# Optimization experiments

Measured on AMD Instinct MI355X. Metric: run time of the kernel, lower is better.

Reference implementation:

```python
import jax, jax.numpy as jnp
import numpy as np

B, NE, NO, D = 8, 1024, 8, 1024
E, K, H = 8, 2, 2048          # num_experts, top-k, expert hidden
O = 1024                      # output_dim
NH, HD = 8, O // 8            # cross-attn heads, head dim
FH = 4 * O                    # ffn hidden


def setup_inputs() -> dict:
    key = jax.random.key(0)
    ks = jax.random.split(key, 24)
    s = lambda i, shape, fan: jax.random.normal(ks[i], shape, jnp.float32) * (1.0 / np.sqrt(fan))
    return {
        "x": jax.random.normal(ks[0], (B, NE, NO, D), jnp.float32),
        "attn_w": s(1, (D,), D),                 # Linear(D,1,bias=False)
        "gate_W": s(2, (D, E), D), "gate_b": jnp.zeros((E,), jnp.float32),
        "eW1": s(3, (E, D, H), D), "eb1": jnp.zeros((E, H), jnp.float32),
        "eW2": s(4, (E, H, O), H), "eb2": jnp.zeros((E, O), jnp.float32),
        "Wq": s(5, (O, O), O), "bq": jnp.zeros((O,), jnp.float32),
        "Wk": s(6, (O, O), O), "bk": jnp.zeros((O,), jnp.float32),
        "Wv": s(7, (O, O), O), "bv": jnp.zeros((O,), jnp.float32),
        "Wo": s(8, (O, O), O), "bo": jnp.zeros((O,), jnp.float32),
        "fW1": s(9, (O, FH), O), "fb1": jnp.zeros((FH,), jnp.float32),
        "fW2": s(10, (FH, O), FH), "fb2": jnp.zeros((O,), jnp.float32),
    }


def reference(x, attn_w, gate_W, gate_b, eW1, eb1, eW2, eb2,
              Wq, bq, Wk, bk, Wv, bv, Wo, bo, fW1, fb1, fW2, fb2):
    # 1) entity-level attention pooling over objects
    logits = jnp.einsum("bnod,d->bno", x, attn_w)          # (B,NE,NO)
    w = jax.nn.softmax(logits, axis=2)
    x_agg = jnp.einsum("bnod,bno->bnd", x, w)              # (B,NE,D)
    xt = x_agg.reshape(B * NE, D)                          # tokens

    # 2) MoE: top-k sparse routing + expert MLPs
    probs = jax.nn.softmax(xt @ gate_W + gate_b, axis=-1)  # (T,E)
    topv, topi = jax.lax.top_k(probs, K)
    gates = topv / jnp.sum(topv, axis=-1, keepdims=True)   # renormalize top-k
    T = xt.shape[0]
    w_full = jnp.zeros((T, E), xt.dtype).at[jnp.arange(T)[:, None], topi].set(gates)
    moe_out = jnp.zeros((T, O), xt.dtype)
    for e in range(E):  # small fixed loop over experts
        h = jax.nn.relu(xt @ eW1[e] + eb1[e])
        moe_out = moe_out + w_full[:, e:e + 1] * (h @ eW2[e] + eb2[e])
    ent = moe_out.reshape(B, NE, O)

    # 3) cross-attention (context=None -> self-attention)
    def split(t):
        return t.reshape(B, NE, NH, HD).transpose(0, 2, 1, 3)
    q = split(ent @ Wq + bq)
    k = split(ent @ Wk + bk)
    v = split(ent @ Wv + bv)
    scores = jnp.einsum("bhnd,bhmd->bhnm", q, k) / np.sqrt(HD).astype(np.float32)
    attn = jax.nn.softmax(scores, axis=-1)
    ctx = jnp.einsum("bhnm,bhmd->bhnd", attn, v)
    rel = ctx.transpose(0, 2, 1, 3).reshape(B, NE, O) @ Wo + bo

    # 4) FFN (dropout is identity in eval)
    return jax.nn.relu(rel @ fW1 + fb1) @ fW2 + fb2
```

## Files before the change

### kernel.cpp

```cpp
#include <hip/hip_runtime.h>
#include <hip/hip_bf16.h>
#include <math.h>


typedef __bf16 bf16_t;
typedef __bf16 bf16x8 __attribute__((ext_vector_type(8)));
typedef float  f32x4  __attribute__((ext_vector_type(4)));

#define B_   8
#define NE_  1024
#define NO_  8
#define D_   1024
#define E_   8
#define H_   2048
#define O_   1024
#define NH_  8
#define HD_  128
#define FH_  4096
#define T_   8192
#define NRB_ 32
#define NBLK_ 136
#define SLOTS_ (NBLK_*128)

__device__ __forceinline__ void gl2lds16(const bf16_t* g, bf16_t* l) {
    __builtin_amdgcn_global_load_lds(
        (const __attribute__((address_space(1))) unsigned int*)g,
        (__attribute__((address_space(3))) unsigned int*)l,
        16, 0, 0);
}

template<typename OUT_T, bool TRANSC, bool BIAS, bool RELU, bool GROUPED, bool GATHER>
__global__ __launch_bounds__(256, 2)
void gemm_nt(const bf16_t* __restrict__ A, const bf16_t* __restrict__ Bm,
             OUT_T* __restrict__ C,
             const float* __restrict__ bias,
             const int* __restrict__ rowidx, const int* __restrict__ blkexp,
             int K, int lda, int ldb, int ldc, float alpha, int zbase,
             long sBe, int biasStride,
             long sAb, long sAh, long sAz,
             long sBb, long sBh, long sBz,
             long sCb, long sCh, long sCz)
{
    const int z  = blockIdx.z;
    const long bh = zbase + z;
    const long bb = bh >> 3, hh = bh & 7;
    A  += bb*sAb + hh*sAh + (long)z*sAz;
    Bm += bb*sBb + hh*sBh + (long)z*sBz;
    C  += bb*sCb + hh*sCh + (long)z*sCz;

    if (GROUPED) {
        const int ge = blkexp[blockIdx.x];
        if (ge < 0) return;
        Bm += (long)ge * sBe;
        if (BIAS) bias += (long)ge * biasStride;
    }

    __shared__ __align__(16) bf16_t As[128*32];
    __shared__ __align__(16) bf16_t Bs[128*32];

    const int t    = threadIdx.x;
    const int lane = t & 63, wave = t >> 6;
    const int l16  = lane & 15, quad = lane >> 4;
    const int wm   = (wave & 1) * 64, wn = (wave >> 1) * 64;
    const int rowBase = blockIdx.x * 128;
    const int colBase = blockIdx.y * 128;

    const int lrow = lane >> 2;
    const int lch  = (lane & 3) * 8;
    long arow0, arow1;
    if (GATHER) {
        arow0 = rowidx[rowBase + wave*16 + lrow];
        arow1 = rowidx[rowBase + wave*16 + lrow + 64];
    } else {
        arow0 = rowBase + wave*16 + lrow;
        arow1 = arow0 + 64;
    }
    const bf16_t* agp0 = A  + arow0*lda + lch;
    const bf16_t* agp1 = A  + arow1*lda + lch;
    const bf16_t* bgp0 = Bm + (long)(colBase + wave*16 + lrow)*ldb + lch;
    const bf16_t* bgp1 = bgp0 + (long)64*ldb;
    bf16_t* alp0 = &As[wave*512];
    bf16_t* alp1 = &As[(4 + wave)*512];
    bf16_t* blp0 = &Bs[wave*512];
    bf16_t* blp1 = &Bs[(4 + wave)*512];

    f32x4 acc[4][4] = {};

    for (int k0 = 0; k0 < K; k0 += 32) {
        __syncthreads();
        gl2lds16(agp0 + k0, alp0);
        gl2lds16(agp1 + k0, alp1);
        gl2lds16(bgp0 + k0, blp0);
        gl2lds16(bgp1 + k0, blp1);
        __syncthreads();

        bf16x8 af[4], bfr[4];
        #pragma unroll
        for (int mi = 0; mi < 4; mi++)
            af[mi] = *(const bf16x8*)&As[(wm + mi*16 + l16)*32 + quad*8];
        #pragma unroll
        for (int ni = 0; ni < 4; ni++)
            bfr[ni] = *(const bf16x8*)&Bs[(wn + ni*16 + l16)*32 + quad*8];
        #pragma unroll
        for (int mi = 0; mi < 4; mi++)
            #pragma unroll
            for (int ni = 0; ni < 4; ni++)
                acc[mi][ni] = __builtin_amdgcn_mfma_f32_16x16x32_bf16(
                                  af[mi], bfr[ni], acc[mi][ni], 0, 0, 0);
    }

    #pragma unroll
    for (int mi = 0; mi < 4; mi++) {
        #pragma unroll
        for (int ni = 0; ni < 4; ni++) {
            const int col = colBase + wn + ni*16 + l16;
            float bv = 0.0f;
            if (BIAS) bv = bias[col];
            #pragma unroll
            for (int rr = 0; rr < 4; rr++) {
                const int row = rowBase + wm + mi*16 + quad*4 + rr;
                float v = acc[mi][ni][rr] * alpha;
                if (BIAS)   v += bv;
                if (RELU)   v = fmaxf(v, 0.0f);
                if (TRANSC) C[(long)col*ldc + row] = (OUT_T)v;
                else        C[(long)row*ldc + col] = (OUT_T)v;
            }
        }
    }
}

__global__ __launch_bounds__(256)
void transpose_convert(const float* __restrict__ in, bf16_t* __restrict__ out,
                       int R, int C, long inStride, long outStride)
{
    __shared__ float tl[64][65];
    const int t = threadIdx.x;
    const float* src = in  + (long)blockIdx.z * inStride;
    bf16_t*      dst = out + (long)blockIdx.z * outStride;
    const int c0 = blockIdx.x * 64, r0 = blockIdx.y * 64;
    #pragma unroll
    for (int i = 0; i < 16; i++) {
        const int idx = t + i*256, r = idx >> 6, c = idx & 63;
        tl[r][c] = src[(long)(r0 + r)*C + c0 + c];
    }
    __syncthreads();
    #pragma unroll
    for (int i = 0; i < 16; i++) {
        const int idx = t + i*256, rT = idx >> 6, cT = idx & 63;
        dst[(long)(c0 + rT)*R + r0 + cT] = (bf16_t)tl[cT][rT];
    }
}

__global__ __launch_bounds__(256)
void pool_kernel(const float* __restrict__ x, const float* __restrict__ attn_w,
                 float* __restrict__ xaggf, bf16_t* __restrict__ xaggb)
{
    __shared__ float xs[8192];
    __shared__ float red[32];
    const int t = threadIdx.x;
    const long tok = blockIdx.x;
    const float4* src = (const float4*)(x + tok*8192);
    float4* xs4 = (float4*)xs;
    #pragma unroll
    for (int i = 0; i < 8; i++) xs4[t + i*256] = src[t + i*256];
    float wreg[4];
    #pragma unroll
    for (int j = 0; j < 4; j++) wreg[j] = attn_w[t + j*256];
    __syncthreads();

    float part[8];
    #pragma unroll
    for (int o = 0; o < 8; o++) {
        float p = 0.0f;
        #pragma unroll
        for (int j = 0; j < 4; j++) p += xs[o*1024 + t + j*256] * wreg[j];
        part[o] = p;
    }
    const int lane = t & 63, wv = t >> 6;
    #pragma unroll
    for (int o = 0; o < 8; o++) {
        float v = part[o];
        for (int off = 32; off; off >>= 1) v += __shfl_down(v, off);
        if (lane == 0) red[o*4 + wv] = v;
    }
    __syncthreads();
    float lg[8], mx = -3.4e38f;
    #pragma unroll
    for (int o = 0; o < 8; o++) {
        lg[o] = red[o*4] + red[o*4+1] + red[o*4+2] + red[o*4+3];
        mx = fmaxf(mx, lg[o]);
    }
    float ssum = 0.0f;
    #pragma unroll
    for (int o = 0; o < 8; o++) { lg[o] = expf(lg[o] - mx); ssum += lg[o]; }
    const float inv = 1.0f / ssum;
    #pragma unroll
    for (int j = 0; j < 4; j++) {
        const int d = t + j*256;
        float a = 0.0f;
        #pragma unroll
        for (int o = 0; o < 8; o++) a += lg[o] * xs[o*1024 + d];
        a *= inv;
        xaggf[tok*1024 + d] = a;
        xaggb[tok*1024 + d] = (bf16_t)a;
    }
}

__global__ __launch_bounds__(256)
void gate_kernel(const float* __restrict__ xaggf, const float* __restrict__ gate_W,
                 const float* __restrict__ gate_b, float* __restrict__ gpair,
                 unsigned int* __restrict__ picks)
{
    const int t = threadIdx.x;
    const int lane = t & 63, wv = t >> 6;
    const long tok = (long)blockIdx.x*4 + wv;
    const float* xr = xaggf + tok*1024;
    float acc[8] = {0,0,0,0,0,0,0,0};
    for (int j = 0; j < 16; j++) {
        const int d = lane + j*64;
        const float xv = xr[d];
        const float4 w0 = *(const float4*)(gate_W + (long)d*8);
        const float4 w1 = *(const float4*)(gate_W + (long)d*8 + 4);
        acc[0] += xv*w0.x; acc[1] += xv*w0.y; acc[2] += xv*w0.z; acc[3] += xv*w0.w;
        acc[4] += xv*w1.x; acc[5] += xv*w1.y; acc[6] += xv*w1.z; acc[7] += xv*w1.w;
    }
    #pragma unroll
    for (int e = 0; e < 8; e++)
        for (int off = 32; off; off >>= 1) acc[e] += __shfl_down(acc[e], off);
    if (lane == 0) {
        float l[8];
        #pragma unroll
        for (int e = 0; e < 8; e++) l[e] = acc[e] + gate_b[e];
        int i1 = 0; float v1 = l[0];
        #pragma unroll
        for (int e = 1; e < 8; e++) if (l[e] > v1) { v1 = l[e]; i1 = e; }
        int i2 = -1; float v2 = -3.4e38f;
        #pragma unroll
        for (int e = 0; e < 8; e++) if (e != i1 && l[e] > v2) { v2 = l[e]; i2 = e; }
        const float tt = expf(v2 - v1);
        gpair[tok*2 + 0] = 1.0f/(1.0f + tt);
        gpair[tok*2 + 1] = tt/(1.0f + tt);
        picks[tok] = (unsigned)(i1 | (i2 << 8));
    }
}

__global__ __launch_bounds__(256)
void route_count(const unsigned int* __restrict__ picks, int* __restrict__ blockcnt)
{
    __shared__ int h[8];
    const int t = threadIdx.x;
    if (t < 8) h[t] = 0;
    __syncthreads();
    const unsigned p = picks[blockIdx.x*256 + t];
    atomicAdd(&h[p & 7], 1);
    atomicAdd(&h[(p >> 8) & 7], 1);
    __syncthreads();
    if (t < 8) blockcnt[blockIdx.x*8 + t] = h[t];
}

__global__ __launch_bounds__(256)
void route_offsets(const int* __restrict__ blockcnt,
                   int* __restrict__ blockbase, int* __restrict__ blkexp)
{
    __shared__ int cntS[8], eoffS[9];
    const int t = threadIdx.x;
    if (t < 8) {
        int s = 0;
        for (int b = 0; b < NRB_; b++) s += blockcnt[b*8 + t];
        cntS[t] = s;
    }
    __syncthreads();
    if (t == 0) {
        int r = 0;
        for (int e = 0; e < 8; e++) { eoffS[e] = r; r += (cntS[e] + 127) & ~127; }
        eoffS[8] = r;
    }
    __syncthreads();
    if (t < 8) {
        int r = eoffS[t];
        for (int b = 0; b < NRB_; b++) { blockbase[b*8 + t] = r; r += blockcnt[b*8 + t]; }
    }
    if (t < NBLK_) {
        const int s = t * 128;
        int e = -1;
        for (int q = 0; q < 8; q++) if (s >= eoffS[q] && s < eoffS[q+1]) e = q;
        blkexp[t] = e;
    }
}

__global__ __launch_bounds__(256)
void route_scatter(const unsigned int* __restrict__ picks,
                   const int* __restrict__ blockbase,
                   int* __restrict__ eidx2, int* __restrict__ tok2slot)
{
    __shared__ int c[8];
    const int t = threadIdx.x;
    if (t < 8) c[t] = 0;
    __syncthreads();
    const int tok = blockIdx.x*256 + t;
    const unsigned p = picks[tok];
    const int e1 = p & 7, e2 = (p >> 8) & 7;
    const int l1 = atomicAdd(&c[e1], 1);
    const int l2 = atomicAdd(&c[e2], 1);
    const int s1 = blockbase[blockIdx.x*8 + e1] + l1;
    const int s2 = blockbase[blockIdx.x*8 + e2] + l2;
    eidx2[s1] = tok;
    eidx2[s2] = tok;
    tok2slot[tok*2 + 0] = s1;
    tok2slot[tok*2 + 1] = s2;
}

__global__ __launch_bounds__(256)
void combine_kernel(const float* __restrict__ out2, const float* __restrict__ gpair,
                    const int* __restrict__ tok2slot, bf16_t* __restrict__ entb)
{
    const int t = threadIdx.x;
    const long tok = blockIdx.x;
    const int s1 = tok2slot[tok*2], s2 = tok2slot[tok*2 + 1];
    const float g1 = gpair[tok*2], g2 = gpair[tok*2 + 1];
    const float4 a = ((const float4*)(out2 + (long)s1*O_))[t];
    const float4 b = ((const float4*)(out2 + (long)s2*O_))[t];
    union { bf16_t h[4]; uint2 u; } pk;
    pk.h[0] = (bf16_t)(g1*a.x + g2*b.x);
    pk.h[1] = (bf16_t)(g1*a.y + g2*b.y);
    pk.h[2] = (bf16_t)(g1*a.z + g2*b.z);
    pk.h[3] = (bf16_t)(g1*a.w + g2*b.w);
    ((uint2*)(entb + tok*O_))[t] = pk.u;
}

__global__ __launch_bounds__(256)
void softmax_rows(float* __restrict__ S)
{
    __shared__ float redA[4], redB[4];
    const int t = threadIdx.x;
    float* rowp = S + (long)blockIdx.x * 1024;
    const float4 v = ((const float4*)rowp)[t];
    const int lane = t & 63, wv = t >> 6;
    float m = fmaxf(fmaxf(v.x, v.y), fmaxf(v.z, v.w));
    for (int off = 32; off; off >>= 1) m = fmaxf(m, __shfl_down(m, off));
    if (lane == 0) redA[wv] = m;
    __syncthreads();
    m = fmaxf(fmaxf(redA[0], redA[1]), fmaxf(redA[2], redA[3]));
    const float e0 = expf(v.x - m), e1 = expf(v.y - m);
    const float e2 = expf(v.z - m), e3 = expf(v.w - m);
    float s = e0 + e1 + e2 + e3;
    for (int off = 32; off; off >>= 1) s += __shfl_down(s, off);
    if (lane == 0) redB[wv] = s;
    __syncthreads();
    const float inv = 1.0f / (redB[0] + redB[1] + redB[2] + redB[3]);
    union { bf16_t h[4]; uint2 u; } pk;
    pk.h[0] = (bf16_t)(e0*inv); pk.h[1] = (bf16_t)(e1*inv);
    pk.h[2] = (bf16_t)(e2*inv); pk.h[3] = (bf16_t)(e3*inv);
    ((uint2*)rowp)[t] = pk.u;
}

extern "C" void kernel_launch(void* const* d_in, const int* in_sizes, int n_in,
                              void* d_out, int out_size, void* d_ws, size_t ws_size,
                              hipStream_t stream)
{
    const float* x      = (const float*)d_in[0];
    const float* attn_w = (const float*)d_in[1];
    const float* gate_W = (const float*)d_in[2];
    const float* gate_b = (const float*)d_in[3];
    const float* eW1    = (const float*)d_in[4];
    const float* eb1    = (const float*)d_in[5];
    const float* eW2    = (const float*)d_in[6];
    const float* eb2    = (const float*)d_in[7];
    const float* Wq     = (const float*)d_in[8];   const float* bq = (const float*)d_in[9];
    const float* Wk     = (const float*)d_in[10];  const float* bk = (const float*)d_in[11];
    const float* Wv     = (const float*)d_in[12];  const float* bv = (const float*)d_in[13];
    const float* Wo     = (const float*)d_in[14];  const float* bo = (const float*)d_in[15];
    const float* fW1    = (const float*)d_in[16];  const float* fb1 = (const float*)d_in[17];
    const float* fW2    = (const float*)d_in[18];  const float* fb2 = (const float*)d_in[19];
    float* out = (float*)d_out;

    char* ws = (char*)d_ws;
    size_t off = 0;
    auto alloc = [&](size_t sz) -> void* {
        void* p = (void*)(ws + off);
        off += (sz + 255) & ~(size_t)255;
        return p;
    };
    bf16_t* WqT  = (bf16_t*)alloc((size_t)O_*O_*2);
    bf16_t* WkT  = (bf16_t*)alloc((size_t)O_*O_*2);
    bf16_t* WvT  = (bf16_t*)alloc((size_t)O_*O_*2);
    bf16_t* WoT  = (bf16_t*)alloc((size_t)O_*O_*2);
    bf16_t* fW1T = (bf16_t*)alloc((size_t)O_*FH_*2);
    bf16_t* fW2T = (bf16_t*)alloc((size_t)FH_*O_*2);
    bf16_t* eW1T = (bf16_t*)alloc((size_t)E_*D_*H_*2);
    bf16_t* eW2T = (bf16_t*)alloc((size_t)E_*H_*O_*2);
    unsigned int* picks = (unsigned int*)alloc((size_t)T_*4);
    float*  gpair    = (float*)alloc((size_t)T_*2*4);
    int*    blockcnt = (int*)alloc((size_t)NRB_*8*4);
    int*    blockbase= (int*)alloc((size_t)NRB_*8*4);
    int*    blkexp   = (int*)alloc((size_t)NBLK_*4);
    int*    eidx2    = (int*)alloc((size_t)SLOTS_*4);
    int*    tok2slot = (int*)alloc((size_t)T_*2*4);
    const size_t reuse0 = off;
    float*  xaggf  = (float*)alloc((size_t)T_*D_*4);
    bf16_t* xaggb  = (bf16_t*)alloc((size_t)T_*D_*2);
    bf16_t* hidden = (bf16_t*)alloc((size_t)SLOTS_*H_*2);
    bf16_t* entb   = (bf16_t*)alloc((size_t)T_*O_*2);
    bf16_t* qb     = (bf16_t*)alloc((size_t)T_*O_*2);
    bf16_t* kb     = (bf16_t*)alloc((size_t)T_*O_*2);
    bf16_t* vT     = (bf16_t*)alloc((size_t)O_*T_*2);
    float*  S      = (float*)alloc((size_t)16*NE_*NE_*4);
    bf16_t* ctxb   = (bf16_t*)alloc((size_t)T_*O_*2);
    float*  out2  = (float*)S;
    bf16_t* ffnhb = (bf16_t*)(ws + reuse0);
    bf16_t* relb  = (bf16_t*)(ws + reuse0 + (size_t)80*1024*1024);

    const dim3 blk(256);

    transpose_convert<<<dim3(H_/64, D_/64, E_), blk, 0, stream>>>(eW1, eW1T, D_, H_, (long)D_*H_, (long)D_*H_);
    transpose_convert<<<dim3(O_/64, H_/64, E_), blk, 0, stream>>>(eW2, eW2T, H_, O_, (long)H_*O_, (long)H_*O_);
    transpose_convert<<<dim3(O_/64, O_/64, 1), blk, 0, stream>>>(Wq, WqT, O_, O_, 0, 0);
    transpose_convert<<<dim3(O_/64, O_/64, 1), blk, 0, stream>>>(Wk, WkT, O_, O_, 0, 0);
    transpose_convert<<<dim3(O_/64, O_/64, 1), blk, 0, stream>>>(Wv, WvT, O_, O_, 0, 0);
    transpose_convert<<<dim3(O_/64, O_/64, 1), blk, 0, stream>>>(Wo, WoT, O_, O_, 0, 0);
    transpose_convert<<<dim3(FH_/64, O_/64, 1), blk, 0, stream>>>(fW1, fW1T, O_, FH_, 0, 0);
    transpose_convert<<<dim3(O_/64, FH_/64, 1), blk, 0, stream>>>(fW2, fW2T, FH_, O_, 0, 0);

    (void)hipMemsetAsync(eidx2, 0, (size_t)SLOTS_*4, stream);
    pool_kernel<<<dim3(T_), blk, 0, stream>>>(x, attn_w, xaggf, xaggb);
    gate_kernel<<<dim3(T_/4), blk, 0, stream>>>(xaggf, gate_W, gate_b, gpair, picks);
    route_count  <<<dim3(NRB_), blk, 0, stream>>>(picks, blockcnt);
    route_offsets<<<dim3(1),    blk, 0, stream>>>(blockcnt, blockbase, blkexp);
    route_scatter<<<dim3(NRB_), blk, 0, stream>>>(picks, blockbase, eidx2, tok2slot);

    gemm_nt<bf16_t, false, true, true, true, true><<<dim3(NBLK_, 16, 1), blk, 0, stream>>>(
        xaggb, eW1T, hidden, eb1, eidx2, blkexp,
        D_, D_, D_, H_, 1.0f, 0, (long)D_*H_, H_, 0,0,0, 0,0,0, 0,0,0);
    gemm_nt<float, false, true, false, true, false><<<dim3(NBLK_, 8, 1), blk, 0, stream>>>(
        hidden, eW2T, out2, eb2, nullptr, blkexp,
        H_, H_, H_, O_, 1.0f, 0, (long)H_*O_, O_, 0,0,0, 0,0,0, 0,0,0);
    combine_kernel<<<dim3(T_), blk, 0, stream>>>(out2, gpair, tok2slot, entb);

    gemm_nt<bf16_t, false, true, false, false, false><<<dim3(64, 8, 1), blk, 0, stream>>>(
        entb, WqT, qb, bq, nullptr, nullptr, O_, O_, O_, O_, 1.0f, 0, 0,0, 0,0,0, 0,0,0, 0,0,0);
    gemm_nt<bf16_t, false, true, false, false, false><<<dim3(64, 8, 1), blk, 0, stream>>>(
        entb, WkT, kb, bk, nullptr, nullptr, O_, O_, O_, O_, 1.0f, 0, 0,0, 0,0,0, 0,0,0, 0,0,0);
    gemm_nt<bf16_t, true, true, false, false, false><<<dim3(64, 8, 1), blk, 0, stream>>>(
        entb, WvT, vT, bv, nullptr, nullptr, O_, O_, O_, T_, 1.0f, 0, 0,0, 0,0,0, 0,0,0, 0,0,0);

    const float scl = 0.088388347648318447f;
    for (int c = 0; c < 4; c++) {
        const int zb = c * 16;
        gemm_nt<float, false, false, false, false, false><<<dim3(8, 8, 16), blk, 0, stream>>>(
            qb, kb, S, nullptr, nullptr, nullptr, HD_, O_, O_, NE_, scl, zb, 0,0,
            (long)NE_*O_, HD_, 0,   (long)NE_*O_, HD_, 0,   0, 0, (long)NE_*NE_);
        softmax_rows<<<dim3(16*NE_), blk, 0, stream>>>(S);
        gemm_nt<bf16_t, false, false, false, false, false><<<dim3(8, 1, 16), blk, 0, stream>>>(
            (const bf16_t*)S, vT, ctxb, nullptr, nullptr, nullptr, NE_, 2*NE_, T_, O_, 1.0f, zb, 0,0,
            0, 0, (long)2*NE_*NE_,   (long)NE_, (long)HD_*T_, 0,   (long)NE_*O_, HD_, 0);
    }

    gemm_nt<bf16_t, false, true, false, false, false><<<dim3(64, 8, 1), blk, 0, stream>>>(
        ctxb, WoT, relb, bo, nullptr, nullptr, O_, O_, O_, O_, 1.0f, 0, 0,0, 0,0,0, 0,0,0, 0,0,0);
    gemm_nt<bf16_t, false, true, true, false, false><<<dim3(64, 32, 1), blk, 0, stream>>>(
        relb, fW1T, ffnhb, fb1, nullptr, nullptr, O_, O_, O_, FH_, 1.0f, 0, 0,0, 0,0,0, 0,0,0, 0,0,0);
    gemm_nt<float, false, true, false, false, false><<<dim3(64, 8, 1), blk, 0, stream>>>(
        ffnhb, fW2T, out, fb2, nullptr, nullptr, FH_, FH_, FH_, O_, 1.0f, 0, 0,0, 0,0,0, 0,0,0, 0,0,0);
}
```

Baseline: 1.373 ms.

## Fuse attention into flash-attention kernel and merge pooling with gating

Replaces the chunked QK^T GEMM, row softmax and PV GEMM sequence with one flash-attention kernel. It uses online softmax, keeps scores in registers and LDS, and reuses the K buffer to stage P. This removes the float score-matrix round trips to global memory and twelve kernel launches. Separately, the gate projection and top-2 selection are folded into the pooling kernel, so the float copy of pooled tokens is no longer written and re-read. The trade-off is heavier register use per block, which is bounded to two blocks per CU, and 64 KB of LDS per block.

```diff
diff --git a/kernel.cpp b/kernel.cpp
--- a/kernel.cpp
+++ b/kernel.cpp
@@ -129,6 +129,158 @@
     }
 }
 
+__global__ __launch_bounds__(256, 2)
+void flash_attn(const bf16_t* __restrict__ qg, const bf16_t* __restrict__ kg,
+                const bf16_t* __restrict__ vTg, bf16_t* __restrict__ ctx)
+{
+    const int bh = blockIdx.z;
+    const long bb = bh >> 3, hh = bh & 7;
+    const int qb0 = blockIdx.x * 128;
+
+    __shared__ __align__(16) bf16_t KP[128*128];
+    __shared__ __align__(16) bf16_t Vs[128*128];
+
+    const int t = threadIdx.x;
+    const int lane = t & 63, w = t >> 6;
+    const int l16 = lane & 15, quad = lane >> 4;
+    const float scl = 0.088388347648318447f;
+
+    bf16x8 qf[2][4];
+    {
+        const bf16_t* q0 = qg + ((long)bb*1024 + qb0 + w*32 + l16)*O_ + hh*128 + quad*8;
+        #pragma unroll
+        for (int mi = 0; mi < 2; mi++)
+            #pragma unroll
+            for (int kk = 0; kk < 4; kk++)
+                qf[mi][kk] = *(const bf16x8*)(q0 + (long)mi*16*O_ + kk*32);
+    }
+
+    f32x4 o[2][8] = {};
+    float mrow[2][4], lrow[2][4];
+    #pragma unroll
+    for (int mi = 0; mi < 2; mi++)
+        #pragma unroll
+        for (int rr = 0; rr < 4; rr++) { mrow[mi][rr] = -3.4e38f; lrow[mi][rr] = 0.0f; }
+
+    const int srloc = lane >> 4;
+    const int spc   = lane & 15;
+
+    for (int kt = 0; kt < 8; kt++) {
+        const int kv0 = kt * 128;
+        __syncthreads();
+
+        #pragma unroll
+        for (int i = 0; i < 8; i++) {
+            const int r = w*32 + i*4 + srloc;
+            const int sc = spc ^ (r & 7);
+            gl2lds16(kg + ((long)bb*1024 + kv0 + r)*O_ + hh*128 + sc*8,
+                     &KP[(w*32 + i*4)*128]);
+            gl2lds16(vTg + ((long)hh*128 + r)*T_ + bb*1024 + kv0 + sc*8,
+                     &Vs[(w*32 + i*4)*128]);
+        }
+        __syncthreads();
+
+        f32x4 sa[2][8] = {};
+        #pragma unroll
+        for (int kk = 0; kk < 4; kk++) {
+            bf16x8 bf_[8];
+            #pragma unroll
+            for (int ni = 0; ni < 8; ni++) {
+                const int n = ni*16 + l16;
+                bf_[ni] = *(const bf16x8*)&KP[n*128 + ((kk*32 + quad*8) ^ ((n & 7) << 3))];
+            }
+            #pragma unroll
+            for (int mi = 0; mi < 2; mi++)
+                #pragma unroll
+                for (int ni = 0; ni < 8; ni++)
+                    sa[mi][ni] = __builtin_amdgcn_mfma_f32_16x16x32_bf16(
+                                     qf[mi][kk], bf_[ni], sa[mi][ni], 0, 0, 0);
+        }
+
+        float f2[2][4];
+        #pragma unroll
+        for (int mi = 0; mi < 2; mi++) {
+            #pragma unroll
+            for (int rr = 0; rr < 4; rr++) {
+                float rm = -3.4e38f;
+                #pragma unroll
+                for (int ni = 0; ni < 8; ni++) rm = fmaxf(rm, sa[mi][ni][rr]);
+                rm *= scl;
+                #pragma unroll
+                for (int off = 1; off < 16; off <<= 1)
+                    rm = fmaxf(rm, __shfl_xor(rm, off));
+                const float mn = fmaxf(mrow[mi][rr], rm);
+                const float f = expf(mrow[mi][rr] - mn);
+                mrow[mi][rr] = mn; f2[mi][rr] = f;
+                float rs = 0.0f;
+                #pragma unroll
+                for (int ni = 0; ni < 8; ni++) {
+                    const float p = expf(sa[mi][ni][rr]*scl - mn);
+                    sa[mi][ni][rr] = p;
+                    rs += p;
+                }
+                #pragma unroll
+                for (int off = 1; off < 16; off <<= 1)
+                    rs += __shfl_xor(rs, off);
+                lrow[mi][rr] = lrow[mi][rr]*f + rs;
+            }
+        }
+        #pragma unroll
+        for (int mi = 0; mi < 2; mi++)
+            #pragma unroll
+            for (int dn = 0; dn < 8; dn++)
+                #pragma unroll
+                for (int rr = 0; rr < 4; rr++)
+                    o[mi][dn][rr] *= f2[mi][rr];
+
+        __syncthreads();
+
+        #pragma unroll
+        for (int mi = 0; mi < 2; mi++)
+            #pragma unroll
+            for (int ni = 0; ni < 8; ni++)
+                #pragma unroll
+                for (int rr = 0; rr < 4; rr++) {
+                    const int qr  = w*32 + mi*16 + quad*4 + rr;
+                    const int col = ni*16 + l16;
+                    KP[qr*128 + (col ^ ((qr & 7) << 3))] = (bf16_t)sa[mi][ni][rr];
+                }
+
+        #pragma unroll
+        for (int kkv = 0; kkv < 4; kkv++) {
+            bf16x8 pa[2], vb[8];
+            #pragma unroll
+            for (int pmi = 0; pmi < 2; pmi++) {
+                const int qr2 = w*32 + pmi*16 + l16;
+                pa[pmi] = *(const bf16x8*)&KP[qr2*128 + ((kkv*32 + quad*8) ^ ((qr2 & 7) << 3))];
+            }
+            #pragma unroll
+            for (int dn = 0; dn < 8; dn++) {
+                const int d = dn*16 + l16;
+                vb[dn] = *(const bf16x8*)&Vs[d*128 + ((kkv*32 + quad*8) ^ ((d & 7) << 3))];
+            }
+            #pragma unroll
+            for (int pmi = 0; pmi < 2; pmi++)
+                #pragma unroll
+                for (int dn = 0; dn < 8; dn++)
+                    o[pmi][dn] = __builtin_amdgcn_mfma_f32_16x16x32_bf16(
+                                     pa[pmi], vb[dn], o[pmi][dn], 0, 0, 0);
+        }
+    }
+
+    #pragma unroll
+    for (int mi = 0; mi < 2; mi++) {
+        #pragma unroll
+        for (int rr = 0; rr < 4; rr++) {
+            const float inv = 1.0f / lrow[mi][rr];
+            const long row = (long)bb*1024 + qb0 + w*32 + mi*16 + quad*4 + rr;
+            #pragma unroll
+            for (int dn = 0; dn < 8; dn++)
+                ctx[row*O_ + hh*128 + dn*16 + l16] = (bf16_t)(o[mi][dn][rr] * inv);
+        }
+    }
+}
+
 __global__ __launch_bounds__(256)
 void transpose_convert(const float* __restrict__ in, bf16_t* __restrict__ out,
                        int R, int C, long inStride, long outStride)
@@ -152,8 +304,10 @@
 }
 
 __global__ __launch_bounds__(256)
-void pool_kernel(const float* __restrict__ x, const float* __restrict__ attn_w,
-                 float* __restrict__ xaggf, bf16_t* __restrict__ xaggb)
+void pool_gate_kernel(const float* __restrict__ x, const float* __restrict__ attn_w,
+                      const float* __restrict__ gate_W, const float* __restrict__ gate_b,
+                      bf16_t* __restrict__ xaggb, float* __restrict__ gpair,
+                      unsigned int* __restrict__ picks)
 {
     __shared__ float xs[8192];
     __shared__ float red[32];
@@ -194,6 +348,8 @@
     #pragma unroll
     for (int o = 0; o < 8; o++) { lg[o] = expf(lg[o] - mx); ssum += lg[o]; }
     const float inv = 1.0f / ssum;
+
+    float gl[8] = {0,0,0,0,0,0,0,0};
     #pragma unroll
     for (int j = 0; j < 4; j++) {
         const int d = t + j*256;
@@ -201,36 +357,25 @@
         #pragma unroll
         for (int o = 0; o < 8; o++) a += lg[o] * xs[o*1024 + d];
         a *= inv;
-        xaggf[tok*1024 + d] = a;
         xaggb[tok*1024 + d] = (bf16_t)a;
-    }
-}
-
-__global__ __launch_bounds__(256)
-void gate_kernel(const float* __restrict__ xaggf, const float* __restrict__ gate_W,
-                 const float* __restrict__ gate_b, float* __restrict__ gpair,
-                 unsigned int* __restrict__ picks)
-{
-    const int t = threadIdx.x;
-    const int lane = t & 63, wv = t >> 6;
-    const long tok = (long)blockIdx.x*4 + wv;
-    const float* xr = xaggf + tok*1024;
-    float acc[8] = {0,0,0,0,0,0,0,0};
-    for (int j = 0; j < 16; j++) {
-        const int d = lane + j*64;
-        const float xv = xr[d];
         const float4 w0 = *(const float4*)(gate_W + (long)d*8);
         const float4 w1 = *(const float4*)(gate_W + (long)d*8 + 4);
-        acc[0] += xv*w0.x; acc[1] += xv*w0.y; acc[2] += xv*w0.z; acc[3] += xv*w0.w;
-        acc[4] += xv*w1.x; acc[5] += xv*w1.y; acc[6] += xv*w1.z; acc[7] += xv*w1.w;
-    }
-    #pragma unroll
-    for (int e = 0; e < 8; e++)
-        for (int off = 32; off; off >>= 1) acc[e] += __shfl_down(acc[e], off);
-    if (lane == 0) {
+        gl[0] += a*w0.x; gl[1] += a*w0.y; gl[2] += a*w0.z; gl[3] += a*w0.w;
+        gl[4] += a*w1.x; gl[5] += a*w1.y; gl[6] += a*w1.z; gl[7] += a*w1.w;
+    }
+    __syncthreads();
+    #pragma unroll
+    for (int e = 0; e < 8; e++) {
+        float v = gl[e];
+        for (int off = 32; off; off >>= 1) v += __shfl_down(v, off);
+        if (lane == 0) red[e*4 + wv] = v;
+    }
+    __syncthreads();
+    if (t == 0) {
         float l[8];
         #pragma unroll
-        for (int e = 0; e < 8; e++) l[e] = acc[e] + gate_b[e];
+        for (int e = 0; e < 8; e++)
+            l[e] = red[e*4] + red[e*4+1] + red[e*4+2] + red[e*4+3] + gate_b[e];
         int i1 = 0; float v1 = l[0];
         #pragma unroll
         for (int e = 1; e < 8; e++) if (l[e] > v1) { v1 = l[e]; i1 = e; }
@@ -326,32 +471,6 @@
     pk.h[2] = (bf16_t)(g1*a.z + g2*b.z);
     pk.h[3] = (bf16_t)(g1*a.w + g2*b.w);
     ((uint2*)(entb + tok*O_))[t] = pk.u;
-}
-
-__global__ __launch_bounds__(256)
-void softmax_rows(float* __restrict__ S)
-{
-    __shared__ float redA[4], redB[4];
-    const int t = threadIdx.x;
-    float* rowp = S + (long)blockIdx.x * 1024;
-    const float4 v = ((const float4*)rowp)[t];
-    const int lane = t & 63, wv = t >> 6;
-    float m = fmaxf(fmaxf(v.x, v.y), fmaxf(v.z, v.w));
-    for (int off = 32; off; off >>= 1) m = fmaxf(m, __shfl_down(m, off));
-    if (lane == 0) redA[wv] = m;
-    __syncthreads();
-    m = fmaxf(fmaxf(redA[0], redA[1]), fmaxf(redA[2], redA[3]));
-    const float e0 = expf(v.x - m), e1 = expf(v.y - m);
-    const float e2 = expf(v.z - m), e3 = expf(v.w - m);
-    float s = e0 + e1 + e2 + e3;
-    for (int off = 32; off; off >>= 1) s += __shfl_down(s, off);
-    if (lane == 0) redB[wv] = s;
-    __syncthreads();
-    const float inv = 1.0f / (redB[0] + redB[1] + redB[2] + redB[3]);
-    union { bf16_t h[4]; uint2 u; } pk;
-    pk.h[0] = (bf16_t)(e0*inv); pk.h[1] = (bf16_t)(e1*inv);
-    pk.h[2] = (bf16_t)(e2*inv); pk.h[3] = (bf16_t)(e3*inv);
-    ((uint2*)rowp)[t] = pk.u;
 }
 
 extern "C" void kernel_launch(void* const* d_in, const int* in_sizes, int n_in,
@@ -397,18 +516,16 @@
     int*    eidx2    = (int*)alloc((size_t)SLOTS_*4);
     int*    tok2slot = (int*)alloc((size_t)T_*2*4);
     const size_t reuse0 = off;
-    float*  xaggf  = (float*)alloc((size_t)T_*D_*4);
     bf16_t* xaggb  = (bf16_t*)alloc((size_t)T_*D_*2);
     bf16_t* hidden = (bf16_t*)alloc((size_t)SLOTS_*H_*2);
+    float*  out2   = (float*)alloc((size_t)SLOTS_*O_*4);
     bf16_t* entb   = (bf16_t*)alloc((size_t)T_*O_*2);
     bf16_t* qb     = (bf16_t*)alloc((size_t)T_*O_*2);
     bf16_t* kb     = (bf16_t*)alloc((size_t)T_*O_*2);
     bf16_t* vT     = (bf16_t*)alloc((size_t)O_*T_*2);
-    float*  S      = (float*)alloc((size_t)16*NE_*NE_*4);
     bf16_t* ctxb   = (bf16_t*)alloc((size_t)T_*O_*2);
-    float*  out2  = (float*)S;
     bf16_t* ffnhb = (bf16_t*)(ws + reuse0);
-    bf16_t* relb  = (bf16_t*)(ws + reuse0 + (size_t)80*1024*1024);
+    bf16_t* relb  = (bf16_t*)(ws + reuse0 + (size_t)64*1024*1024);
 
     const dim3 blk(256);
 
@@ -422,8 +539,8 @@
     transpose_convert<<<dim3(O_/64, FH_/64, 1), blk, 0, stream>>>(fW2, fW2T, FH_, O_, 0, 0);
 
     (void)hipMemsetAsync(eidx2, 0, (size_t)SLOTS_*4, stream);
-    pool_kernel<<<dim3(T_), blk, 0, stream>>>(x, attn_w, xaggf, xaggb);
-    gate_kernel<<<dim3(T_/4), blk, 0, stream>>>(xaggf, gate_W, gate_b, gpair, picks);
+    pool_gate_kernel<<<dim3(T_), blk, 0, stream>>>(x, attn_w, gate_W, gate_b,
+                                                   xaggb, gpair, picks);
     route_count  <<<dim3(NRB_), blk, 0, stream>>>(picks, blockcnt);
     route_offsets<<<dim3(1),    blk, 0, stream>>>(blockcnt, blockbase, blkexp);
     route_scatter<<<dim3(NRB_), blk, 0, stream>>>(picks, blockbase, eidx2, tok2slot);
@@ -443,17 +560,7 @@
     gemm_nt<bf16_t, true, true, false, false, false><<<dim3(64, 8, 1), blk, 0, stream>>>(
         entb, WvT, vT, bv, nullptr, nullptr, O_, O_, O_, T_, 1.0f, 0, 0,0, 0,0,0, 0,0,0, 0,0,0);
 
-    const float scl = 0.088388347648318447f;
-    for (int c = 0; c < 4; c++) {
-        const int zb = c * 16;
-        gemm_nt<float, false, false, false, false, false><<<dim3(8, 8, 16), blk, 0, stream>>>(
-            qb, kb, S, nullptr, nullptr, nullptr, HD_, O_, O_, NE_, scl, zb, 0,0,
-            (long)NE_*O_, HD_, 0,   (long)NE_*O_, HD_, 0,   0, 0, (long)NE_*NE_);
-        softmax_rows<<<dim3(16*NE_), blk, 0, stream>>>(S);
-        gemm_nt<bf16_t, false, false, false, false, false><<<dim3(8, 1, 16), blk, 0, stream>>>(
-            (const bf16_t*)S, vT, ctxb, nullptr, nullptr, nullptr, NE_, 2*NE_, T_, O_, 1.0f, zb, 0,0,
-            0, 0, (long)2*NE_*NE_,   (long)NE_, (long)HD_*T_, 0,   (long)NE_*O_, HD_, 0);
-    }
+    flash_attn<<<dim3(8, 1, 64), blk, 0, stream>>>(qb, kb, vT, ctxb);
 
     gemm_nt<bf16_t, false, true, false, false, false><<<dim3(64, 8, 1), blk, 0, stream>>>(
         ctxb, WoT, relb, bo, nullptr, nullptr, O_, O_, O_, O_, 1.0f, 0, 0,0, 0,0,0, 0,0,0, 0,0,0);
```

Measured after the change: 1.344 ms. 1.02x faster.
